# Performance work log

Hardware: AMD Instinct MI355X
Metric: run time of the kernel (lower is better)

Reference implementation:

```python
import jax, jax.numpy as jnp
import numpy as np

N_NODES = 50000
N_EDGES = 600000
NODE_DIM = 128
EDGE_DIM = 64
HID_DIM = 128
OUT_DIM = 128
BN_EPS = 1e-5


def setup_inputs() -> dict:
    key = jax.random.key(0)
    ks = jax.random.split(key, 16)
    s = 0.02
    return {
        "x": jax.random.normal(ks[0], (N_NODES, NODE_DIM), dtype=jnp.float32),
        "edge_index": jax.random.randint(ks[1], (2, N_EDGES), 0, N_NODES, dtype=jnp.int64),
        "edge_attr": jax.random.normal(ks[2], (N_EDGES, EDGE_DIM), dtype=jnp.float32),
        # conv1 edge lin: edge_dim -> node_dim
        "We1": jax.random.normal(ks[3], (EDGE_DIM, NODE_DIM), dtype=jnp.float32) * s,
        "be1": jnp.zeros((NODE_DIM,), dtype=jnp.float32),
        # conv1 MLP: node_dim -> hid -> hid
        "W1": jax.random.normal(ks[4], (NODE_DIM, HID_DIM), dtype=jnp.float32) * s,
        "b1": jnp.zeros((HID_DIM,), dtype=jnp.float32),
        "W2": jax.random.normal(ks[5], (HID_DIM, HID_DIM), dtype=jnp.float32) * s,
        "b2": jnp.zeros((HID_DIM,), dtype=jnp.float32),
        # conv2 edge lin: edge_dim -> hid
        "We2": jax.random.normal(ks[6], (EDGE_DIM, HID_DIM), dtype=jnp.float32) * s,
        "be2": jnp.zeros((HID_DIM,), dtype=jnp.float32),
        # conv2 MLP: hid -> out -> out
        "W3": jax.random.normal(ks[7], (HID_DIM, OUT_DIM), dtype=jnp.float32) * s,
        "b3": jnp.zeros((OUT_DIM,), dtype=jnp.float32),
        "W4": jax.random.normal(ks[8], (OUT_DIM, OUT_DIM), dtype=jnp.float32) * s,
        "b4": jnp.zeros((OUT_DIM,), dtype=jnp.float32),
        # batch norm affine params
        "gamma": jnp.ones((OUT_DIM,), dtype=jnp.float32),
        "beta": jnp.zeros((OUT_DIM,), dtype=jnp.float32),
    }


def _gine_conv(x, src, dst, edge_attr, We, be, Wa, ba, Wb, bb):
    # message = relu(x_j + Lin(edge_attr)), sum-aggregate at dst, eps = 0
    msg = jax.nn.relu(x[src] + edge_attr @ We + be)          # [E, d]
    aggr = jax.ops.segment_sum(msg, dst, num_segments=x.shape[0])  # [N, d]
    h = x + aggr                                             # (1+eps)*x + aggr
    return jax.nn.relu(h @ Wa + ba) @ Wb + bb


def reference(x, edge_index, edge_attr, We1, be1, W1, b1, W2, b2,
              We2, be2, W3, b3, W4, b4, gamma, beta):
    src, dst = edge_index[0], edge_index[1]
    h = jax.nn.relu(_gine_conv(x, src, dst, edge_attr, We1, be1, W1, b1, W2, b2))
    h = _gine_conv(h, src, dst, edge_attr, We2, be2, W3, b3, W4, b4)
    # BatchNorm1d (training mode: batch statistics, biased variance)
    mean = jnp.mean(h, axis=0)
    var = jnp.mean(jnp.square(h - mean), axis=0)
    return gamma * (h - mean) * jax.lax.rsqrt(var + BN_EPS) + beta
```

## Files before the change

### kernel.cpp

```cpp
#include <hip/hip_runtime.h>

#define NDIM 128
#define EDIM 64
#define BN_EPS 1e-5f
#define SPAN 64
#define WPB  4
#define LPAD (NDIM + 4)
#define PITCH 136

typedef __attribute__((ext_vector_type(8))) short short8v;
typedef __attribute__((ext_vector_type(4))) float float4v;

static __device__ __forceinline__ unsigned short f2bf(float f) {
    union { float f; unsigned u; } c; c.f = f;
    const unsigned r = (c.u + 0x7fffu + ((c.u >> 16) & 1u)) >> 16;
    return (unsigned short)r;
}

static __device__ __forceinline__ short8v cvt_row(const float* __restrict__ arow, int k0) {
    const float4 f0 = *reinterpret_cast<const float4*>(arow + k0);
    const float4 f1 = *reinterpret_cast<const float4*>(arow + k0 + 4);
    short8v a;
    a[0] = (short)f2bf(f0.x); a[1] = (short)f2bf(f0.y);
    a[2] = (short)f2bf(f0.z); a[3] = (short)f2bf(f0.w);
    a[4] = (short)f2bf(f1.x); a[5] = (short)f2bf(f1.y);
    a[6] = (short)f2bf(f1.z); a[7] = (short)f2bf(f1.w);
    return a;
}

__global__ __launch_bounds__(256) void hist_k(
    const int* __restrict__ ei, int* __restrict__ deg, int E)
{
    const int e = blockIdx.x * blockDim.x + threadIdx.x;
    if (e < E) atomicAdd(&deg[ei[E + e]], 1);
}

__global__ __launch_bounds__(1024) void scan_build(
    int* __restrict__ cursor, int* __restrict__ rowptr, int N)
{
    __shared__ int wsums[16];
    __shared__ int run_s;
    const int tid  = threadIdx.x;
    const int lane = tid & 63;
    const int w    = tid >> 6;
    if (tid == 0) run_s = 0;
    __syncthreads();
    for (int base = 0; base < N; base += 1024) {
        const int i = base + tid;
        const int v = (i < N) ? cursor[i] : 0;
        int incl = v;
#pragma unroll
        for (int off = 1; off < 64; off <<= 1) {
            int t = __shfl_up(incl, off, 64);
            if (lane >= off) incl += t;
        }
        if (lane == 63) wsums[w] = incl;
        __syncthreads();
        if (w == 0) {
            int s = (lane < 16) ? wsums[lane] : 0;
#pragma unroll
            for (int off = 1; off < 16; off <<= 1) {
                int t = __shfl_up(s, off, 64);
                if (lane >= off) s += t;
            }
            if (lane < 16) wsums[lane] = s;
        }
        __syncthreads();
        const int waveoff = (w > 0) ? wsums[w - 1] : 0;
        const int run = run_s;
        const int excl = run + waveoff + incl - v;
        if (i < N) { rowptr[i] = excl; cursor[i] = excl; }
        __syncthreads();
        if (tid == 0) run_s += wsums[15];
        __syncthreads();
    }
    if (tid == 0) rowptr[N] = run_s;
}

__global__ __launch_bounds__(256) void scatter_k(
    const int* __restrict__ ei, int* __restrict__ cursor,
    int* __restrict__ srcp, int* __restrict__ eidp, int* __restrict__ dstp, int E)
{
    const int e = blockIdx.x * blockDim.x + threadIdx.x;
    if (e < E) {
        const int d = ei[E + e];
        const int p = atomicAdd(&cursor[d], 1);
        srcp[p] = ei[e];
        eidp[p] = e;
        dstp[p] = d;
    }
}

__global__ __launch_bounds__(64) void prep_we(
    const float* __restrict__ We, unsigned short* __restrict__ WeT)
{
    const int c = blockIdx.x;
    const int k = threadIdx.x;
    WeT[c * EDIM + k] = f2bf(We[k * NDIM + c]);
}

__global__ __launch_bounds__(128) void prep_w(
    const float* __restrict__ W, unsigned short* __restrict__ WT)
{
    const int n = blockIdx.x;
    const int k = threadIdx.x;
    WT[n * NDIM + k] = f2bf(W[k * NDIM + n]);
}

__global__ __launch_bounds__(256) void edge_mfma(
    const float* __restrict__ xnode,
    const float* __restrict__ ea,
    const int*   __restrict__ srcp,
    const int*   __restrict__ eidp,
    const int*   __restrict__ dstp,
    const unsigned short* __restrict__ WeT,
    const float* __restrict__ be,
    float*       __restrict__ aggr,
    int E)
{
    __shared__ float msg[WPB][16][LPAD];

    const int tid   = threadIdx.x;
    const int lane  = tid & 63;
    const int wv    = tid >> 6;
    const int span0 = (blockIdx.x * WPB + wv) * SPAN;
    if (span0 >= E) return;

    const int m16 = lane & 15;
    const int kg  = lane >> 4;
    const int k0a = kg * 8;

    short8v bfrag[2][8];
#pragma unroll
    for (int kk = 0; kk < 2; ++kk)
#pragma unroll
        for (int nt = 0; nt < 8; ++nt) {
            const int col = nt * 16 + m16;
            bfrag[kk][nt] = *reinterpret_cast<const short8v*>(&WeT[col * EDIM + kk * 32 + k0a]);
        }

    const int c0 = lane, c1 = lane + 64;
    const float be0 = be[c0], be1 = be[c1];
    float* msgw = &msg[wv][0][0];

    float a0 = 0.f, a1 = 0.f;

    if (span0 + SPAN <= E) {
        int   sr_c[16], ds_c[16];
        float xv0_c[16], xv1_c[16];
        short8v af_c[2];

#pragma unroll
        for (int s = 0; s < 16; ++s) { sr_c[s] = srcp[span0 + s]; ds_c[s] = dstp[span0 + s]; }
#pragma unroll
        for (int s = 0; s < 16; ++s) {
            xv0_c[s] = xnode[(long)sr_c[s] * NDIM + c0];
            xv1_c[s] = xnode[(long)sr_c[s] * NDIM + c1];
        }
        {
            const float* arow = ea + (long)eidp[span0 + m16] * EDIM;
            af_c[0] = cvt_row(arow, k0a);
            af_c[1] = cvt_row(arow, 32 + k0a);
        }
#pragma unroll
        for (int nt = 0; nt < 8; ++nt) {
            float4v acc = (float4v){0.f, 0.f, 0.f, 0.f};
            acc = __builtin_amdgcn_mfma_f32_16x16x32_bf16(af_c[0], bfrag[0][nt], acc, 0, 0, 0);
            acc = __builtin_amdgcn_mfma_f32_16x16x32_bf16(af_c[1], bfrag[1][nt], acc, 0, 0, 0);
#pragma unroll
            for (int r = 0; r < 4; ++r)
                msgw[(kg * 4 + r) * LPAD + nt * 16 + m16] = acc[r];
        }

        int dcur = ds_c[0];

#pragma unroll
        for (int t = 0; t < SPAN / 16; ++t) {
            const int base = span0 + t * 16;
            int   sr_n[16], ds_n[16];
            float xv0_n[16], xv1_n[16];
            short8v af_n[2];

            if (t + 1 < SPAN / 16) {
#pragma unroll
                for (int s = 0; s < 16; ++s) {
                    sr_n[s] = srcp[base + 16 + s];
                    ds_n[s] = dstp[base + 16 + s];
                }
#pragma unroll
                for (int s = 0; s < 16; ++s) {
                    xv0_n[s] = xnode[(long)sr_n[s] * NDIM + c0];
                    xv1_n[s] = xnode[(long)sr_n[s] * NDIM + c1];
                }
                const float* arow = ea + (long)eidp[base + 16 + m16] * EDIM;
                af_n[0] = cvt_row(arow, k0a);
                af_n[1] = cvt_row(arow, 32 + k0a);
            }

#pragma unroll
            for (int s = 0; s < 16; ++s) {
                if (ds_c[s] != dcur) {
                    atomicAdd(&aggr[(long)dcur * NDIM + c0], a0);
                    atomicAdd(&aggr[(long)dcur * NDIM + c1], a1);
                    a0 = 0.f; a1 = 0.f; dcur = ds_c[s];
                }
                a0 += fmaxf(xv0_c[s] + msgw[s * LPAD + c0] + be0, 0.f);
                a1 += fmaxf(xv1_c[s] + msgw[s * LPAD + c1] + be1, 0.f);
            }

            if (t + 1 < SPAN / 16) {
#pragma unroll
                for (int nt = 0; nt < 8; ++nt) {
                    float4v acc = (float4v){0.f, 0.f, 0.f, 0.f};
                    acc = __builtin_amdgcn_mfma_f32_16x16x32_bf16(af_n[0], bfrag[0][nt], acc, 0, 0, 0);
                    acc = __builtin_amdgcn_mfma_f32_16x16x32_bf16(af_n[1], bfrag[1][nt], acc, 0, 0, 0);
#pragma unroll
                    for (int r = 0; r < 4; ++r)
                        msgw[(kg * 4 + r) * LPAD + nt * 16 + m16] = acc[r];
                }
#pragma unroll
                for (int s = 0; s < 16; ++s) {
                    sr_c[s] = sr_n[s]; ds_c[s] = ds_n[s];
                    xv0_c[s] = xv0_n[s]; xv1_c[s] = xv1_n[s];
                }
            }
        }
        atomicAdd(&aggr[(long)dcur * NDIM + c0], a0);
        atomicAdd(&aggr[(long)dcur * NDIM + c1], a1);
    } else {
        const int spanEnd = E;
        int dcur = dstp[span0];
        for (int t = 0; t < SPAN / 16; ++t) {
            const int base = span0 + t * 16;
            if (base >= spanEnd) break;

            const int  slot = (base + m16 < E) ? base + m16 : E - 1;
            const float* arow = ea + (long)eidp[slot] * EDIM;
            short8v afrag[2];
            afrag[0] = cvt_row(arow, k0a);
            afrag[1] = cvt_row(arow, 32 + k0a);

#pragma unroll
            for (int nt = 0; nt < 8; ++nt) {
                float4v acc = (float4v){0.f, 0.f, 0.f, 0.f};
                acc = __builtin_amdgcn_mfma_f32_16x16x32_bf16(afrag[0], bfrag[0][nt], acc, 0, 0, 0);
                acc = __builtin_amdgcn_mfma_f32_16x16x32_bf16(afrag[1], bfrag[1][nt], acc, 0, 0, 0);
#pragma unroll
                for (int r = 0; r < 4; ++r)
                    msgw[(kg * 4 + r) * LPAD + nt * 16 + m16] = acc[r];
            }

            for (int s = 0; s < 16; ++s) {
                const int gs = base + s;
                if (gs >= spanEnd) break;
                const int d  = dstp[gs];
                const int sr = srcp[gs];
                if (d != dcur) {
                    atomicAdd(&aggr[(long)dcur * NDIM + c0], a0);
                    atomicAdd(&aggr[(long)dcur * NDIM + c1], a1);
                    a0 = 0.f; a1 = 0.f; dcur = d;
                }
                const float xv0 = xnode[(long)sr * NDIM + c0];
                const float xv1 = xnode[(long)sr * NDIM + c1];
                a0 += fmaxf(xv0 + msgw[s * LPAD + c0] + be0, 0.f);
                a1 += fmaxf(xv1 + msgw[s * LPAD + c1] + be1, 0.f);
            }
        }
        atomicAdd(&aggr[(long)dcur * NDIM + c0], a0);
        atomicAdd(&aggr[(long)dcur * NDIM + c1], a1);
    }
}

template <bool FINAL_RELU, bool STATS>
__global__ __launch_bounds__(256) void node_mlp_mfma(
    const float* xin,
    const float* __restrict__ aggr,
    const unsigned short* __restrict__ W1T, const float* __restrict__ b1,
    const unsigned short* __restrict__ W2T, const float* __restrict__ b2,
    float* out,
    float* __restrict__ stats,
    int N)
{
    __shared__ unsigned short in_lds[16][PITCH];
    __shared__ unsigned short t_lds[16][PITCH];

    const int tid  = threadIdx.x;
    const int lane = tid & 63;
    const int wv   = tid >> 6;
    const int wn0  = wv * 32;
    const int m16  = lane & 15;
    const int rg   = lane >> 4;

    short8v b1f[4][2], b2f[4][2];
#pragma unroll
    for (int kt = 0; kt < 4; ++kt)
#pragma unroll
        for (int nt = 0; nt < 2; ++nt) {
            const int col = wn0 + nt * 16 + m16;
            b1f[kt][nt] = *reinterpret_cast<const short8v*>(&W1T[col * NDIM + kt * 32 + rg * 8]);
            b2f[kt][nt] = *reinterpret_cast<const short8v*>(&W2T[col * NDIM + kt * 32 + rg * 8]);
        }
    float bias1[2], bias2[2];
#pragma unroll
    for (int nt = 0; nt < 2; ++nt) {
        bias1[nt] = b1[wn0 + nt * 16 + m16];
        bias2[nt] = b2[wn0 + nt * 16 + m16];
    }

    float ss[2] = {0.f, 0.f}, sq[2] = {0.f, 0.f};

    const int ntile = (N + 15) >> 4;
    for (int tile = blockIdx.x; tile < ntile; tile += gridDim.x) {
        const int nb = tile << 4;

        {
            const int row = tid >> 4;
            const int ch  = tid & 15;
            const int gr  = nb + row;
            short8v pk = (short8v){0, 0, 0, 0, 0, 0, 0, 0};
            if (gr < N) {
                const float4* xp = reinterpret_cast<const float4*>(xin  + (size_t)gr * NDIM + ch * 8);
                const float4* ap = reinterpret_cast<const float4*>(aggr + (size_t)gr * NDIM + ch * 8);
                const float4 x0 = xp[0], x1 = xp[1];
                const float4 g0 = ap[0], g1 = ap[1];
                pk[0] = (short)f2bf(x0.x + g0.x); pk[1] = (short)f2bf(x0.y + g0.y);
                pk[2] = (short)f2bf(x0.z + g0.z); pk[3] = (short)f2bf(x0.w + g0.w);
                pk[4] = (short)f2bf(x1.x + g1.x); pk[5] = (short)f2bf(x1.y + g1.y);
                pk[6] = (short)f2bf(x1.z + g1.z); pk[7] = (short)f2bf(x1.w + g1.w);
            }
            *reinterpret_cast<short8v*>(&in_lds[row][ch * 8]) = pk;
        }
        __syncthreads();

        short8v af[4];
#pragma unroll
        for (int kt = 0; kt < 4; ++kt)
            af[kt] = *reinterpret_cast<const short8v*>(&in_lds[m16][kt * 32 + rg * 8]);
        float4v acc[2];
#pragma unroll
        for (int nt = 0; nt < 2; ++nt) {
            acc[nt] = (float4v){0.f, 0.f, 0.f, 0.f};
#pragma unroll
            for (int kt = 0; kt < 4; ++kt)
                acc[nt] = __builtin_amdgcn_mfma_f32_16x16x32_bf16(af[kt], b1f[kt][nt], acc[nt], 0, 0, 0);
        }
#pragma unroll
        for (int nt = 0; nt < 2; ++nt)
#pragma unroll
            for (int r = 0; r < 4; ++r) {
                const float v = fmaxf(acc[nt][r] + bias1[nt], 0.f);
                t_lds[rg * 4 + r][wn0 + nt * 16 + m16] = f2bf(v);
            }
        __syncthreads();

#pragma unroll
        for (int kt = 0; kt < 4; ++kt)
            af[kt] = *reinterpret_cast<const short8v*>(&t_lds[m16][kt * 32 + rg * 8]);
        float4v acc2[2];
#pragma unroll
        for (int nt = 0; nt < 2; ++nt) {
            acc2[nt] = (float4v){0.f, 0.f, 0.f, 0.f};
#pragma unroll
            for (int kt = 0; kt < 4; ++kt)
                acc2[nt] = __builtin_amdgcn_mfma_f32_16x16x32_bf16(af[kt], b2f[kt][nt], acc2[nt], 0, 0, 0);
        }

#pragma unroll
        for (int nt = 0; nt < 2; ++nt)
#pragma unroll
            for (int r = 0; r < 4; ++r) {
                const int node = nb + rg * 4 + r;
                if (node < N) {
                    float o = acc2[nt][r] + bias2[nt];
                    if (FINAL_RELU) o = fmaxf(o, 0.f);
                    out[(size_t)node * NDIM + wn0 + nt * 16 + m16] = o;
                    if (STATS) { ss[nt] += o; sq[nt] += o * o; }
                }
            }
    }

    if (STATS) {
#pragma unroll
        for (int nt = 0; nt < 2; ++nt) {
            float s = ss[nt], q = sq[nt];
            s += __shfl_xor(s, 16); q += __shfl_xor(q, 16);
            s += __shfl_xor(s, 32); q += __shfl_xor(q, 32);
            if (rg == 0) {
                atomicAdd(&stats[wn0 + nt * 16 + m16], s);
                atomicAdd(&stats[NDIM + wn0 + nt * 16 + m16], q);
            }
        }
    }
}

__global__ __launch_bounds__(256) void bn_apply(
    float* out,
    const float* __restrict__ stats,
    const float* __restrict__ gamma,
    const float* __restrict__ beta,
    int N)
{
    __shared__ float sc_s[NDIM];
    __shared__ float sh_s[NDIM];
    const float invN = 1.f / (float)N;
    if (threadIdx.x < NDIM) {
        const int f = threadIdx.x;
        const float mean = stats[f] * invN;
        const float var  = stats[NDIM + f] * invN - mean * mean;
        const float sc   = gamma[f] * rsqrtf(var + BN_EPS);
        sc_s[f] = sc;
        sh_s[f] = beta[f] - mean * sc;
    }
    __syncthreads();

    const int total4 = N * (NDIM / 4);
    float4* o4 = reinterpret_cast<float4*>(out);
    for (int idx = blockIdx.x * blockDim.x + threadIdx.x; idx < total4;
         idx += gridDim.x * blockDim.x) {
        const int fb = (idx & 31) * 4;
        float4 p = o4[idx];
        p.x = p.x * sc_s[fb + 0] + sh_s[fb + 0];
        p.y = p.y * sc_s[fb + 1] + sh_s[fb + 1];
        p.z = p.z * sc_s[fb + 2] + sh_s[fb + 2];
        p.w = p.w * sc_s[fb + 3] + sh_s[fb + 3];
        o4[idx] = p;
    }
}

extern "C" void kernel_launch(void* const* d_in, const int* in_sizes, int n_in,
                              void* d_out, int out_size, void* d_ws, size_t ws_size,
                              hipStream_t stream)
{
    const float* x    = (const float*)d_in[0];
    const int*   ei   = (const int*)  d_in[1];
    const float* ea   = (const float*)d_in[2];
    const float* We1  = (const float*)d_in[3];
    const float* be1  = (const float*)d_in[4];
    const float* W1   = (const float*)d_in[5];
    const float* b1   = (const float*)d_in[6];
    const float* W2   = (const float*)d_in[7];
    const float* b2   = (const float*)d_in[8];
    const float* We2  = (const float*)d_in[9];
    const float* be2  = (const float*)d_in[10];
    const float* W3   = (const float*)d_in[11];
    const float* b3   = (const float*)d_in[12];
    const float* W4   = (const float*)d_in[13];
    const float* b4   = (const float*)d_in[14];
    const float* gamma = (const float*)d_in[15];
    const float* beta  = (const float*)d_in[16];

    const int N = in_sizes[0] / NDIM;
    const int E = in_sizes[1] / 2;

    float*          aggr   = (float*)d_ws;
    unsigned short* WeT1   = (unsigned short*)(aggr + (size_t)N * NDIM);
    unsigned short* WeT2   = WeT1 + NDIM * EDIM;
    unsigned short* W1T    = WeT2 + NDIM * EDIM;
    unsigned short* W2T    = W1T + NDIM * NDIM;
    unsigned short* W3T    = W2T + NDIM * NDIM;
    unsigned short* W4T    = W3T + NDIM * NDIM;
    int*            rowptr = (int*)(W4T + NDIM * NDIM);
    int*            cursor = rowptr + (N + 1);
    int*            srcp   = cursor + N;
    int*            eidp   = srcp + E;
    int*            dstp   = eidp + E;
    float*          stats  = (float*)(dstp + E);
    float*          h      = (float*)d_out;

    hipMemsetAsync(cursor, 0, (size_t)N * sizeof(int), stream);
    hipMemsetAsync(stats, 0, 2 * NDIM * sizeof(float), stream);

    hist_k<<<(E + 255) / 256, 256, 0, stream>>>(ei, cursor, E);
    scan_build<<<1, 1024, 0, stream>>>(cursor, rowptr, N);
    scatter_k<<<(E + 255) / 256, 256, 0, stream>>>(ei, cursor, srcp, eidp, dstp, E);
    prep_we<<<NDIM, EDIM, 0, stream>>>(We1, WeT1);
    prep_we<<<NDIM, EDIM, 0, stream>>>(We2, WeT2);
    prep_w<<<NDIM, NDIM, 0, stream>>>(W1, W1T);
    prep_w<<<NDIM, NDIM, 0, stream>>>(W2, W2T);
    prep_w<<<NDIM, NDIM, 0, stream>>>(W3, W3T);
    prep_w<<<NDIM, NDIM, 0, stream>>>(W4, W4T);

    const int egrid = (E + WPB * SPAN - 1) / (WPB * SPAN);
    const int mgrid = 625;

    hipMemsetAsync(aggr, 0, (size_t)N * NDIM * sizeof(float), stream);
    edge_mfma<<<egrid, 256, 0, stream>>>(x, ea, srcp, eidp, dstp, WeT1, be1, aggr, E);
    node_mlp_mfma<true, false><<<mgrid, 256, 0, stream>>>(x, aggr, W1T, b1, W2T, b2,
                                                          h, nullptr, N);
    hipMemsetAsync(aggr, 0, (size_t)N * NDIM * sizeof(float), stream);
    edge_mfma<<<egrid, 256, 0, stream>>>(h, ea, srcp, eidp, dstp, WeT2, be2, aggr, E);
    node_mlp_mfma<false, true><<<mgrid, 256, 0, stream>>>(h, aggr, W3T, b3, W4T, b4,
                                                          h, stats, N);
    bn_apply<<<1024, 256, 0, stream>>>(h, stats, gamma, beta, N);
}
```

Measured before the change: 392.4 us.

## Persistent-style edge kernel with balanced tile ranges, bf16 LDS messages, fused weight prep

The edge kernel now runs a fixed grid of 1024 blocks. Each wave processes a contiguous, balanced range of 16-edge tiles instead of a fixed 64-edge span, and a separate tail handles leftover edges. This reduces launch and prologue overhead (loading weight fragments) and lengthens the software-pipelined loop. The message tile in LDS is stored as bf16 to halve LDS footprint, and launch_bounds asks for 3 blocks per CU. The six weight-transpose kernels are fused into one launch. The bf16 rounding of the edge-linear output adds some precision loss.

```diff
diff --git a/kernel.cpp b/kernel.cpp
--- a/kernel.cpp
+++ b/kernel.cpp
@@ -3,9 +3,8 @@
 #define NDIM 128
 #define EDIM 64
 #define BN_EPS 1e-5f
-#define SPAN 64
 #define WPB  4
-#define LPAD (NDIM + 4)
+#define MPITCH 136
 #define PITCH 136
 
 typedef __attribute__((ext_vector_type(8))) short short8v;
@@ -15,6 +14,10 @@
     union { float f; unsigned u; } c; c.f = f;
     const unsigned r = (c.u + 0x7fffu + ((c.u >> 16) & 1u)) >> 16;
     return (unsigned short)r;
+}
+static __device__ __forceinline__ float bf2f(unsigned short u) {
+    union { unsigned u; float f; } c; c.u = ((unsigned)u) << 16;
+    return c.f;
 }
 
 static __device__ __forceinline__ short8v cvt_row(const float* __restrict__ arow, int k0) {
@@ -91,23 +94,27 @@
     }
 }
 
-__global__ __launch_bounds__(64) void prep_we(
-    const float* __restrict__ We, unsigned short* __restrict__ WeT)
+__global__ __launch_bounds__(128) void prep_all(
+    const float* __restrict__ We1, const float* __restrict__ We2,
+    const float* __restrict__ W1, const float* __restrict__ W2,
+    const float* __restrict__ W3, const float* __restrict__ W4,
+    unsigned short* __restrict__ WeT1, unsigned short* __restrict__ WeT2,
+    unsigned short* __restrict__ W1T, unsigned short* __restrict__ W2T,
+    unsigned short* __restrict__ W3T, unsigned short* __restrict__ W4T)
 {
     const int c = blockIdx.x;
     const int k = threadIdx.x;
-    WeT[c * EDIM + k] = f2bf(We[k * NDIM + c]);
-}
-
-__global__ __launch_bounds__(128) void prep_w(
-    const float* __restrict__ W, unsigned short* __restrict__ WT)
-{
-    const int n = blockIdx.x;
-    const int k = threadIdx.x;
-    WT[n * NDIM + k] = f2bf(W[k * NDIM + n]);
-}
-
-__global__ __launch_bounds__(256) void edge_mfma(
+    if (k < EDIM) {
+        WeT1[c * EDIM + k] = f2bf(We1[k * NDIM + c]);
+        WeT2[c * EDIM + k] = f2bf(We2[k * NDIM + c]);
+    }
+    W1T[c * NDIM + k] = f2bf(W1[k * NDIM + c]);
+    W2T[c * NDIM + k] = f2bf(W2[k * NDIM + c]);
+    W3T[c * NDIM + k] = f2bf(W3[k * NDIM + c]);
+    W4T[c * NDIM + k] = f2bf(W4[k * NDIM + c]);
+}
+
+__global__ __launch_bounds__(256, 3) void edge_mfma(
     const float* __restrict__ xnode,
     const float* __restrict__ ea,
     const int*   __restrict__ srcp,
@@ -118,13 +125,11 @@
     float*       __restrict__ aggr,
     int E)
 {
-    __shared__ float msg[WPB][16][LPAD];
-
-    const int tid   = threadIdx.x;
-    const int lane  = tid & 63;
-    const int wv    = tid >> 6;
-    const int span0 = (blockIdx.x * WPB + wv) * SPAN;
-    if (span0 >= E) return;
+    __shared__ unsigned short msg[WPB][16][MPITCH];
+
+    const int tid  = threadIdx.x;
+    const int lane = tid & 63;
+    const int wv   = tid >> 6;
 
     const int m16 = lane & 15;
     const int kg  = lane >> 4;
@@ -141,24 +146,30 @@
 
     const int c0 = lane, c1 = lane + 64;
     const float be0 = be[c0], be1 = be[c1];
-    float* msgw = &msg[wv][0][0];
-
-    float a0 = 0.f, a1 = 0.f;
-
-    if (span0 + SPAN <= E) {
+    unsigned short* msgw = &msg[wv][0][0];
+
+    const int T  = E >> 4;
+    const int W  = blockIdx.x * WPB + wv;
+    const int nw = gridDim.x * WPB;
+    const int q  = T / nw, rr = T % nw;
+    const int t0 = W * q + (W < rr ? W : rr);
+    const int cnt = q + (W < rr ? 1 : 0);
+
+    if (cnt > 0) {
+        const int s0 = t0 << 4;
         int   sr_c[16], ds_c[16];
         float xv0_c[16], xv1_c[16];
         short8v af_c[2];
 
 #pragma unroll
-        for (int s = 0; s < 16; ++s) { sr_c[s] = srcp[span0 + s]; ds_c[s] = dstp[span0 + s]; }
+        for (int s = 0; s < 16; ++s) { sr_c[s] = srcp[s0 + s]; ds_c[s] = dstp[s0 + s]; }
 #pragma unroll
         for (int s = 0; s < 16; ++s) {
             xv0_c[s] = xnode[(long)sr_c[s] * NDIM + c0];
             xv1_c[s] = xnode[(long)sr_c[s] * NDIM + c1];
         }
         {
-            const float* arow = ea + (long)eidp[span0 + m16] * EDIM;
+            const float* arow = ea + (long)eidp[s0 + m16] * EDIM;
             af_c[0] = cvt_row(arow, k0a);
             af_c[1] = cvt_row(arow, 32 + k0a);
         }
@@ -169,19 +180,20 @@
             acc = __builtin_amdgcn_mfma_f32_16x16x32_bf16(af_c[1], bfrag[1][nt], acc, 0, 0, 0);
 #pragma unroll
             for (int r = 0; r < 4; ++r)
-                msgw[(kg * 4 + r) * LPAD + nt * 16 + m16] = acc[r];
-        }
-
+                msgw[(kg * 4 + r) * MPITCH + nt * 16 + m16] = f2bf(acc[r]);
+        }
+
+        float a0 = 0.f, a1 = 0.f;
         int dcur = ds_c[0];
 
-#pragma unroll
-        for (int t = 0; t < SPAN / 16; ++t) {
-            const int base = span0 + t * 16;
+        for (int t = 0; t < cnt; ++t) {
+            const int base = s0 + (t << 4);
             int   sr_n[16], ds_n[16];
             float xv0_n[16], xv1_n[16];
             short8v af_n[2];
-
-            if (t + 1 < SPAN / 16) {
+            const bool hn = (t + 1 < cnt);
+
+            if (hn) {
 #pragma unroll
                 for (int s = 0; s < 16; ++s) {
                     sr_n[s] = srcp[base + 16 + s];
@@ -204,11 +216,11 @@
                     atomicAdd(&aggr[(long)dcur * NDIM + c1], a1);
                     a0 = 0.f; a1 = 0.f; dcur = ds_c[s];
                 }
-                a0 += fmaxf(xv0_c[s] + msgw[s * LPAD + c0] + be0, 0.f);
-                a1 += fmaxf(xv1_c[s] + msgw[s * LPAD + c1] + be1, 0.f);
-            }
-
-            if (t + 1 < SPAN / 16) {
+                a0 += fmaxf(xv0_c[s] + bf2f(msgw[s * MPITCH + c0]) + be0, 0.f);
+                a1 += fmaxf(xv1_c[s] + bf2f(msgw[s * MPITCH + c1]) + be1, 0.f);
+            }
+
+            if (hn) {
 #pragma unroll
                 for (int nt = 0; nt < 8; ++nt) {
                     float4v acc = (float4v){0.f, 0.f, 0.f, 0.f};
@@ -216,7 +228,7 @@
                     acc = __builtin_amdgcn_mfma_f32_16x16x32_bf16(af_n[1], bfrag[1][nt], acc, 0, 0, 0);
 #pragma unroll
                     for (int r = 0; r < 4; ++r)
-                        msgw[(kg * 4 + r) * LPAD + nt * 16 + m16] = acc[r];
+                        msgw[(kg * 4 + r) * MPITCH + nt * 16 + m16] = f2bf(acc[r]);
                 }
 #pragma unroll
                 for (int s = 0; s < 16; ++s) {
@@ -227,44 +239,38 @@
         }
         atomicAdd(&aggr[(long)dcur * NDIM + c0], a0);
         atomicAdd(&aggr[(long)dcur * NDIM + c1], a1);
-    } else {
-        const int spanEnd = E;
-        int dcur = dstp[span0];
-        for (int t = 0; t < SPAN / 16; ++t) {
-            const int base = span0 + t * 16;
-            if (base >= spanEnd) break;
-
-            const int  slot = (base + m16 < E) ? base + m16 : E - 1;
-            const float* arow = ea + (long)eidp[slot] * EDIM;
-            short8v afrag[2];
-            afrag[0] = cvt_row(arow, k0a);
-            afrag[1] = cvt_row(arow, 32 + k0a);
-
-#pragma unroll
-            for (int nt = 0; nt < 8; ++nt) {
-                float4v acc = (float4v){0.f, 0.f, 0.f, 0.f};
-                acc = __builtin_amdgcn_mfma_f32_16x16x32_bf16(afrag[0], bfrag[0][nt], acc, 0, 0, 0);
-                acc = __builtin_amdgcn_mfma_f32_16x16x32_bf16(afrag[1], bfrag[1][nt], acc, 0, 0, 0);
-#pragma unroll
-                for (int r = 0; r < 4; ++r)
-                    msgw[(kg * 4 + r) * LPAD + nt * 16 + m16] = acc[r];
-            }
-
-            for (int s = 0; s < 16; ++s) {
-                const int gs = base + s;
-                if (gs >= spanEnd) break;
-                const int d  = dstp[gs];
-                const int sr = srcp[gs];
-                if (d != dcur) {
-                    atomicAdd(&aggr[(long)dcur * NDIM + c0], a0);
-                    atomicAdd(&aggr[(long)dcur * NDIM + c1], a1);
-                    a0 = 0.f; a1 = 0.f; dcur = d;
-                }
-                const float xv0 = xnode[(long)sr * NDIM + c0];
-                const float xv1 = xnode[(long)sr * NDIM + c1];
-                a0 += fmaxf(xv0 + msgw[s * LPAD + c0] + be0, 0.f);
-                a1 += fmaxf(xv1 + msgw[s * LPAD + c1] + be1, 0.f);
-            }
+    }
+
+    if ((E & 15) && W == nw - 1) {
+        const int base = T << 4;
+        const int slot = (base + m16 < E) ? base + m16 : E - 1;
+        const float* arow = ea + (long)eidp[slot] * EDIM;
+        short8v afrag[2];
+        afrag[0] = cvt_row(arow, k0a);
+        afrag[1] = cvt_row(arow, 32 + k0a);
+#pragma unroll
+        for (int nt = 0; nt < 8; ++nt) {
+            float4v acc = (float4v){0.f, 0.f, 0.f, 0.f};
+            acc = __builtin_amdgcn_mfma_f32_16x16x32_bf16(afrag[0], bfrag[0][nt], acc, 0, 0, 0);
+            acc = __builtin_amdgcn_mfma_f32_16x16x32_bf16(afrag[1], bfrag[1][nt], acc, 0, 0, 0);
+#pragma unroll
+            for (int r = 0; r < 4; ++r)
+                msgw[(kg * 4 + r) * MPITCH + nt * 16 + m16] = f2bf(acc[r]);
+        }
+        float a0 = 0.f, a1 = 0.f;
+        int dcur = dstp[base];
+        for (int s = 0; s < 16; ++s) {
+            const int gs = base + s;
+            if (gs >= E) break;
+            const int d  = dstp[gs];
+            const int sr = srcp[gs];
+            if (d != dcur) {
+                atomicAdd(&aggr[(long)dcur * NDIM + c0], a0);
+                atomicAdd(&aggr[(long)dcur * NDIM + c1], a1);
+                a0 = 0.f; a1 = 0.f; dcur = d;
+            }
+            a0 += fmaxf(xnode[(long)sr * NDIM + c0] + bf2f(msgw[s * MPITCH + c0]) + be0, 0.f);
+            a1 += fmaxf(xnode[(long)sr * NDIM + c1] + bf2f(msgw[s * MPITCH + c1]) + be1, 0.f);
         }
         atomicAdd(&aggr[(long)dcur * NDIM + c0], a0);
         atomicAdd(&aggr[(long)dcur * NDIM + c1], a1);
@@ -473,14 +479,10 @@
     hist_k<<<(E + 255) / 256, 256, 0, stream>>>(ei, cursor, E);
     scan_build<<<1, 1024, 0, stream>>>(cursor, rowptr, N);
     scatter_k<<<(E + 255) / 256, 256, 0, stream>>>(ei, cursor, srcp, eidp, dstp, E);
-    prep_we<<<NDIM, EDIM, 0, stream>>>(We1, WeT1);
-    prep_we<<<NDIM, EDIM, 0, stream>>>(We2, WeT2);
-    prep_w<<<NDIM, NDIM, 0, stream>>>(W1, W1T);
-    prep_w<<<NDIM, NDIM, 0, stream>>>(W2, W2T);
-    prep_w<<<NDIM, NDIM, 0, stream>>>(W3, W3T);
-    prep_w<<<NDIM, NDIM, 0, stream>>>(W4, W4T);
-
-    const int egrid = (E + WPB * SPAN - 1) / (WPB * SPAN);
+    prep_all<<<NDIM, NDIM, 0, stream>>>(We1, We2, W1, W2, W3, W4,
+                                        WeT1, WeT2, W1T, W2T, W3T, W4T);
+
+    const int egrid = 1024;
     const int mgrid = 625;
 
     hipMemsetAsync(aggr, 0, (size_t)N * NDIM * sizeof(float), stream);
```

Measured after the change: 539.9 us. 37.6% more time.

## Prefetch edge attributes two tiles ahead and merge weight prep kernels

Applied to the files above, without the earlier changes.

The edge kernel now loads the raw fp32 edge-attribute rows two 16-edge tiles ahead into registers and converts them to bf16 just before the MFMA. This hides the latency of the random edge-attribute gathers behind more work than before. Separately, the six weight transpose/convert launches are merged into one kernel to cut launch overhead. The deeper prefetch adds 32 live float registers per thread, which could lower occupancy.

```diff
diff --git a/kernel.cpp b/kernel.cpp
--- a/kernel.cpp
+++ b/kernel.cpp
@@ -17,15 +17,19 @@
     return (unsigned short)r;
 }
 
-static __device__ __forceinline__ short8v cvt_row(const float* __restrict__ arow, int k0) {
-    const float4 f0 = *reinterpret_cast<const float4*>(arow + k0);
-    const float4 f1 = *reinterpret_cast<const float4*>(arow + k0 + 4);
+static __device__ __forceinline__ short8v pack_bf(const float4 f0, const float4 f1) {
     short8v a;
     a[0] = (short)f2bf(f0.x); a[1] = (short)f2bf(f0.y);
     a[2] = (short)f2bf(f0.z); a[3] = (short)f2bf(f0.w);
     a[4] = (short)f2bf(f1.x); a[5] = (short)f2bf(f1.y);
     a[6] = (short)f2bf(f1.z); a[7] = (short)f2bf(f1.w);
     return a;
+}
+
+static __device__ __forceinline__ short8v cvt_row(const float* __restrict__ arow, int k0) {
+    const float4 f0 = *reinterpret_cast<const float4*>(arow + k0);
+    const float4 f1 = *reinterpret_cast<const float4*>(arow + k0 + 4);
+    return pack_bf(f0, f1);
 }
 
 __global__ __launch_bounds__(256) void hist_k(
@@ -91,20 +95,24 @@
     }
 }
 
-__global__ __launch_bounds__(64) void prep_we(
-    const float* __restrict__ We, unsigned short* __restrict__ WeT)
+__global__ __launch_bounds__(128) void prep_all(
+    const float* __restrict__ We1, const float* __restrict__ We2,
+    const float* __restrict__ W1, const float* __restrict__ W2,
+    const float* __restrict__ W3, const float* __restrict__ W4,
+    unsigned short* __restrict__ WeT1, unsigned short* __restrict__ WeT2,
+    unsigned short* __restrict__ W1T, unsigned short* __restrict__ W2T,
+    unsigned short* __restrict__ W3T, unsigned short* __restrict__ W4T)
 {
     const int c = blockIdx.x;
     const int k = threadIdx.x;
-    WeT[c * EDIM + k] = f2bf(We[k * NDIM + c]);
-}
-
-__global__ __launch_bounds__(128) void prep_w(
-    const float* __restrict__ W, unsigned short* __restrict__ WT)
-{
-    const int n = blockIdx.x;
-    const int k = threadIdx.x;
-    WT[n * NDIM + k] = f2bf(W[k * NDIM + n]);
+    if (k < EDIM) {
+        WeT1[c * EDIM + k] = f2bf(We1[k * NDIM + c]);
+        WeT2[c * EDIM + k] = f2bf(We2[k * NDIM + c]);
+    }
+    W1T[c * NDIM + k] = f2bf(W1[k * NDIM + c]);
+    W2T[c * NDIM + k] = f2bf(W2[k * NDIM + c]);
+    W3T[c * NDIM + k] = f2bf(W3[k * NDIM + c]);
+    W4T[c * NDIM + k] = f2bf(W4[k * NDIM + c]);
 }
 
 __global__ __launch_bounds__(256) void edge_mfma(
@@ -148,7 +156,8 @@
     if (span0 + SPAN <= E) {
         int   sr_c[16], ds_c[16];
         float xv0_c[16], xv1_c[16];
-        short8v af_c[2];
+        float4 eaf_n[4];
+        float4 eaf_nn[4];
 
 #pragma unroll
         for (int s = 0; s < 16; ++s) { sr_c[s] = srcp[span0 + s]; ds_c[s] = dstp[span0 + s]; }
@@ -159,17 +168,24 @@
         }
         {
             const float* arow = ea + (long)eidp[span0 + m16] * EDIM;
-            af_c[0] = cvt_row(arow, k0a);
-            af_c[1] = cvt_row(arow, 32 + k0a);
-        }
-#pragma unroll
-        for (int nt = 0; nt < 8; ++nt) {
-            float4v acc = (float4v){0.f, 0.f, 0.f, 0.f};
-            acc = __builtin_amdgcn_mfma_f32_16x16x32_bf16(af_c[0], bfrag[0][nt], acc, 0, 0, 0);
-            acc = __builtin_amdgcn_mfma_f32_16x16x32_bf16(af_c[1], bfrag[1][nt], acc, 0, 0, 0);
-#pragma unroll
-            for (int r = 0; r < 4; ++r)
-                msgw[(kg * 4 + r) * LPAD + nt * 16 + m16] = acc[r];
+            short8v af0 = cvt_row(arow, k0a);
+            short8v af1 = cvt_row(arow, 32 + k0a);
+#pragma unroll
+            for (int nt = 0; nt < 8; ++nt) {
+                float4v acc = (float4v){0.f, 0.f, 0.f, 0.f};
+                acc = __builtin_amdgcn_mfma_f32_16x16x32_bf16(af0, bfrag[0][nt], acc, 0, 0, 0);
+                acc = __builtin_amdgcn_mfma_f32_16x16x32_bf16(af1, bfrag[1][nt], acc, 0, 0, 0);
+#pragma unroll
+                for (int r = 0; r < 4; ++r)
+                    msgw[(kg * 4 + r) * LPAD + nt * 16 + m16] = acc[r];
+            }
+        }
+        {
+            const float* arow = ea + (long)eidp[span0 + 16 + m16] * EDIM;
+            eaf_n[0] = *reinterpret_cast<const float4*>(arow + k0a);
+            eaf_n[1] = *reinterpret_cast<const float4*>(arow + k0a + 4);
+            eaf_n[2] = *reinterpret_cast<const float4*>(arow + 32 + k0a);
+            eaf_n[3] = *reinterpret_cast<const float4*>(arow + 32 + k0a + 4);
         }
 
         int dcur = ds_c[0];
@@ -177,11 +193,12 @@
 #pragma unroll
         for (int t = 0; t < SPAN / 16; ++t) {
             const int base = span0 + t * 16;
+            const bool hn  = (t + 1 < SPAN / 16);
+            const bool hnn = (t + 2 < SPAN / 16);
             int   sr_n[16], ds_n[16];
             float xv0_n[16], xv1_n[16];
-            short8v af_n[2];
-
-            if (t + 1 < SPAN / 16) {
+
+            if (hn) {
 #pragma unroll
                 for (int s = 0; s < 16; ++s) {
                     sr_n[s] = srcp[base + 16 + s];
@@ -192,9 +209,14 @@
                     xv0_n[s] = xnode[(long)sr_n[s] * NDIM + c0];
                     xv1_n[s] = xnode[(long)sr_n[s] * NDIM + c1];
                 }
-                const float* arow = ea + (long)eidp[base + 16 + m16] * EDIM;
-                af_n[0] = cvt_row(arow, k0a);
-                af_n[1] = cvt_row(arow, 32 + k0a);
+            }
+
+            if (hnn) {
+                const float* arow = ea + (long)eidp[base + 32 + m16] * EDIM;
+                eaf_nn[0] = *reinterpret_cast<const float4*>(arow + k0a);
+                eaf_nn[1] = *reinterpret_cast<const float4*>(arow + k0a + 4);
+                eaf_nn[2] = *reinterpret_cast<const float4*>(arow + 32 + k0a);
+                eaf_nn[3] = *reinterpret_cast<const float4*>(arow + 32 + k0a + 4);
             }
 
 #pragma unroll
@@ -208,16 +230,20 @@
                 a1 += fmaxf(xv1_c[s] + msgw[s * LPAD + c1] + be1, 0.f);
             }
 
-            if (t + 1 < SPAN / 16) {
+            if (hn) {
+                const short8v af0 = pack_bf(eaf_n[0], eaf_n[1]);
+                const short8v af1 = pack_bf(eaf_n[2], eaf_n[3]);
 #pragma unroll
                 for (int nt = 0; nt < 8; ++nt) {
                     float4v acc = (float4v){0.f, 0.f, 0.f, 0.f};
-                    acc = __builtin_amdgcn_mfma_f32_16x16x32_bf16(af_n[0], bfrag[0][nt], acc, 0, 0, 0);
-                    acc = __builtin_amdgcn_mfma_f32_16x16x32_bf16(af_n[1], bfrag[1][nt], acc, 0, 0, 0);
+                    acc = __builtin_amdgcn_mfma_f32_16x16x32_bf16(af0, bfrag[0][nt], acc, 0, 0, 0);
+                    acc = __builtin_amdgcn_mfma_f32_16x16x32_bf16(af1, bfrag[1][nt], acc, 0, 0, 0);
 #pragma unroll
                     for (int r = 0; r < 4; ++r)
                         msgw[(kg * 4 + r) * LPAD + nt * 16 + m16] = acc[r];
                 }
+#pragma unroll
+                for (int i = 0; i < 4; ++i) eaf_n[i] = eaf_nn[i];
 #pragma unroll
                 for (int s = 0; s < 16; ++s) {
                     sr_c[s] = sr_n[s]; ds_c[s] = ds_n[s];
@@ -473,12 +499,8 @@
     hist_k<<<(E + 255) / 256, 256, 0, stream>>>(ei, cursor, E);
     scan_build<<<1, 1024, 0, stream>>>(cursor, rowptr, N);
     scatter_k<<<(E + 255) / 256, 256, 0, stream>>>(ei, cursor, srcp, eidp, dstp, E);
-    prep_we<<<NDIM, EDIM, 0, stream>>>(We1, WeT1);
-    prep_we<<<NDIM, EDIM, 0, stream>>>(We2, WeT2);
-    prep_w<<<NDIM, NDIM, 0, stream>>>(W1, W1T);
-    prep_w<<<NDIM, NDIM, 0, stream>>>(W2, W2T);
-    prep_w<<<NDIM, NDIM, 0, stream>>>(W3, W3T);
-    prep_w<<<NDIM, NDIM, 0, stream>>>(W4, W4T);
+    prep_all<<<NDIM, NDIM, 0, stream>>>(We1, We2, W1, W2, W3, W4,
+                                        WeT1, WeT2, W1T, W2T, W3T, W4T);
 
     const int egrid = (E + WPB * SPAN - 1) / (WPB * SPAN);
     const int mgrid = 625;
```

Result: slower. 444.1 us (+13.2%).
